# Performance work log

Hardware: AMD Instinct MI355X
Metric: run time of the kernel (lower is better)

The kernel has to match this reference:

```python
import jax, jax.numpy as jnp
import numpy as np

NUM_HEADS = 16
HEAD_DIM = 64
EMBED_DIM = 1024
BSZ = 4
SEQ = 2048


def setup_inputs() -> dict:
    key = jax.random.key(0)
    ks = jax.random.split(key, 6)
    scale = 1.0 / np.sqrt(EMBED_DIM)
    return {
        "x": jax.random.normal(ks[0], (BSZ, SEQ, EMBED_DIM), jnp.float32),
        "rel_pos_bias": jax.random.normal(ks[1], (1, NUM_HEADS, SEQ, SEQ), jnp.float32),
        "Wq": jax.random.normal(ks[2], (EMBED_DIM, EMBED_DIM), jnp.float32) * scale,
        "Wk": jax.random.normal(ks[3], (EMBED_DIM, EMBED_DIM), jnp.float32) * scale,
        "Wv": jax.random.normal(ks[4], (EMBED_DIM, EMBED_DIM), jnp.float32) * scale,
        "Wo": jax.random.normal(ks[5], (EMBED_DIM, EMBED_DIM), jnp.float32) * scale,
    }


def reference(x, rel_pos_bias, Wq, Wk, Wv, Wo):
    b, s, e = x.shape
    h, d = NUM_HEADS, HEAD_DIM
    # projections (T5 linears have no bias); torch Linear: x @ W.T
    q = (x @ Wq.T).reshape(b, s, h, d).transpose(0, 2, 1, 3)  # [b,h,s,d]
    k = (x @ Wk.T).reshape(b, s, h, d).transpose(0, 2, 1, 3)
    v = (x @ Wv.T).reshape(b, s, h, d).transpose(0, 2, 1, 3)
    # unscaled attention scores + additive relative-position bias
    scores = jnp.einsum("bhqd,bhkd->bhqk", q, k) + rel_pos_bias  # [b,h,s,s]
    weights = jax.nn.softmax(scores.astype(jnp.float32), axis=-1).astype(scores.dtype)
    attn = jnp.einsum("bhqk,bhkd->bhqd", weights, v)  # [b,h,s,d]
    attn = attn.transpose(0, 2, 1, 3).reshape(b, s, e)
    return attn @ Wo.T
```

## Files before the change

kernel.cpp:

```cpp
#include <hip/hip_runtime.h>
#include <hip/hip_bf16.h>

#define NH 16
#define HD 64
#define ED 1024
#define BS 4
#define SL 2048

typedef _Float16 f16x8 __attribute__((ext_vector_type(8)));
typedef _Float16 f16x4 __attribute__((ext_vector_type(4)));
typedef _Float16 f16x2 __attribute__((ext_vector_type(2)));
typedef float floatx4 __attribute__((ext_vector_type(4)));

__global__ __launch_bounds__(256) void cvtw_kernel(const float* __restrict__ Wq,
                                                   const float* __restrict__ Wk,
                                                   const float* __restrict__ Wv,
                                                   _Float16* __restrict__ Wh)
{
    const float* W = (blockIdx.y == 0) ? Wq : (blockIdx.y == 1) ? Wk : Wv;
    _Float16* out = Wh + (size_t)blockIdx.y * (ED * ED);
    const int i = (blockIdx.x * 256 + threadIdx.x) * 4;
    float4 v = *(const float4*)(W + i);
    f16x4 c;
    c[0] = (_Float16)v.x; c[1] = (_Float16)v.y;
    c[2] = (_Float16)v.z; c[3] = (_Float16)v.w;
    *(f16x4*)(out + i) = c;
}

__device__ __forceinline__ int lds_boff(int kq, int rc)
{
    return (((kq << 7) + rc) << 4) ^ (kq << 5);
}

template <int A_MODE, int B_MODE, int OUT_MODE>
__device__ __forceinline__ void gemm128_body(const float* __restrict__ Af,
                                             const _Float16* __restrict__ Ah,
                                             const float* __restrict__ Bf,
                                             const _Float16* __restrict__ Bh,
                                             _Float16* __restrict__ outH,
                                             float* __restrict__ outF,
                                             int K, int N)
{
    __shared__ __align__(16) _Float16 As[4 * 128 * 8];
    __shared__ __align__(16) _Float16 Bs[4 * 128 * 8];

    const int tid  = threadIdx.x;
    const int wave = tid >> 6;
    const int lane = tid & 63;
    const int lo16 = lane & 15;
    const int hi4  = lane >> 4;
    const int wm = wave >> 1;
    const int wn = wave & 1;
    const int rowTile = blockIdx.y * 128;
    const int colTile = blockIdx.x * 128;

    floatx4 acc[4][4];
#pragma unroll
    for (int m = 0; m < 4; m++)
#pragma unroll
        for (int n = 0; n < 4; n++)
            acc[m][n] = (floatx4){0.f, 0.f, 0.f, 0.f};

    for (int kb = 0; kb < K; kb += 32) {
        float4 aF[4]; f16x8 aH[2];
        if (A_MODE == 0) {
#pragma unroll
            for (int r = 0; r < 4; r++) {
                const int t2 = tid + r * 256;
                const int row = t2 >> 3;
                const int k4 = (t2 & 7) * 4;
                aF[r] = *(const float4*)(Af + (size_t)(rowTile + row) * K + kb + k4);
            }
        } else {
#pragma unroll
            for (int r = 0; r < 2; r++) {
                const int t2 = tid + r * 256;
                const int row = t2 >> 2;
                const int ko = (t2 & 3) * 8;
                const int gr = rowTile + row;
                const int b = gr >> 11;
                const int s = gr & (SL - 1);
                const int k0 = kb + ko;
                const int h = k0 >> 6;
                const int d = k0 & (HD - 1);
                aH[r] = *(const f16x8*)(Ah + (((size_t)(b * NH + h)) * SL + s) * HD + d);
            }
        }
        f16x8 bH[2]; float4 bF[4];
        if (B_MODE == 0) {
#pragma unroll
            for (int r = 0; r < 2; r++) {
                const int t2 = tid + r * 256;
                const int col = t2 >> 2;
                const int ko = (t2 & 3) * 8;
                bH[r] = *(const f16x8*)(Bh + (size_t)(colTile + col) * K + kb + ko);
            }
        } else {
#pragma unroll
            for (int r = 0; r < 4; r++) {
                const int t2 = tid + r * 256;
                const int col = t2 >> 3;
                const int k4 = (t2 & 7) * 4;
                bF[r] = *(const float4*)(Bf + (size_t)(colTile + col) * K + kb + k4);
            }
        }

        __syncthreads();
        if (A_MODE == 0) {
#pragma unroll
            for (int r = 0; r < 4; r++) {
                const int t2 = tid + r * 256;
                const int row = t2 >> 3;
                const int k4 = (t2 & 7) * 4;
                f16x4 c;
                c[0] = (_Float16)aF[r].x; c[1] = (_Float16)aF[r].y;
                c[2] = (_Float16)aF[r].z; c[3] = (_Float16)aF[r].w;
                *(f16x4*)((char*)As + lds_boff(k4 >> 3, row) + (k4 & 7) * 2) = c;
            }
        } else {
#pragma unroll
            for (int r = 0; r < 2; r++) {
                const int t2 = tid + r * 256;
                const int row = t2 >> 2;
                const int ko = (t2 & 3) * 8;
                *(f16x8*)((char*)As + lds_boff(ko >> 3, row)) = aH[r];
            }
        }
        if (B_MODE == 0) {
#pragma unroll
            for (int r = 0; r < 2; r++) {
                const int t2 = tid + r * 256;
                const int col = t2 >> 2;
                const int ko = (t2 & 3) * 8;
                *(f16x8*)((char*)Bs + lds_boff(ko >> 3, col)) = bH[r];
            }
        } else {
#pragma unroll
            for (int r = 0; r < 4; r++) {
                const int t2 = tid + r * 256;
                const int col = t2 >> 3;
                const int k4 = (t2 & 7) * 4;
                f16x4 c;
                c[0] = (_Float16)bF[r].x; c[1] = (_Float16)bF[r].y;
                c[2] = (_Float16)bF[r].z; c[3] = (_Float16)bF[r].w;
                *(f16x4*)((char*)Bs + lds_boff(k4 >> 3, col) + (k4 & 7) * 2) = c;
            }
        }
        __syncthreads();

        f16x8 af[4], bfr[4];
#pragma unroll
        for (int m = 0; m < 4; m++)
            af[m] = *(const f16x8*)((char*)As + lds_boff(hi4, wm * 64 + m * 16 + lo16));
#pragma unroll
        for (int n = 0; n < 4; n++)
            bfr[n] = *(const f16x8*)((char*)Bs + lds_boff(hi4, wn * 64 + n * 16 + lo16));
#pragma unroll
        for (int m = 0; m < 4; m++)
#pragma unroll
            for (int n = 0; n < 4; n++)
                acc[m][n] = __builtin_amdgcn_mfma_f32_16x16x32_f16(af[m], bfr[n], acc[m][n], 0, 0, 0);
    }

#pragma unroll
    for (int m = 0; m < 4; m++) {
#pragma unroll
        for (int n = 0; n < 4; n++) {
            const int col = colTile + wn * 64 + n * 16 + lo16;
#pragma unroll
            for (int i = 0; i < 4; i++) {
                const int row = rowTile + wm * 64 + m * 16 + hi4 * 4 + i;
                float v = acc[m][n][i];
                if (OUT_MODE == 0) {
                    int b = row >> 11;
                    int s = row & (SL - 1);
                    int h = col >> 6;
                    int d = col & (HD - 1);
                    outH[(((size_t)(b * NH + h)) * SL + s) * HD + d] = (_Float16)v;
                } else {
                    outF[(size_t)row * N + col] = v;
                }
            }
        }
    }
}

__global__ __launch_bounds__(256) void qkv_kernel(const float* __restrict__ x,
                                                  const _Float16* __restrict__ Wh,
                                                  _Float16* __restrict__ Q,
                                                  _Float16* __restrict__ Kk,
                                                  _Float16* __restrict__ V)
{
    const _Float16* W = Wh + (size_t)blockIdx.z * (ED * ED);
    _Float16* out = (blockIdx.z == 0) ? Q : (blockIdx.z == 1) ? Kk : V;
    gemm128_body<0, 0, 0>(x, nullptr, nullptr, W, out, nullptr, ED, ED);
}

__global__ __launch_bounds__(256) void oproj_kernel(const _Float16* __restrict__ A,
                                                    const float* __restrict__ Wo,
                                                    float* __restrict__ out)
{
    gemm128_body<1, 1, 1>(nullptr, A, Wo, nullptr, nullptr, out, ED, ED);
}

__global__ __launch_bounds__(256) void attn_kernel(const _Float16* __restrict__ Qg,
                                                   const _Float16* __restrict__ Kg,
                                                   const _Float16* __restrict__ Vg,
                                                   const float* __restrict__ bias,
                                                   _Float16* __restrict__ attnOut)
{
    __shared__ __align__(16) _Float16 Ks[8 * 64 * 8];
    __shared__ __align__(16) _Float16 Vt[64 * 64];
    __shared__ __align__(16) _Float16 Ps[4 * 32 * 64];
    __shared__ __align__(16) _Float16 Bi[128 * 68];

    const int qt = blockIdx.x;
    const int b  = blockIdx.y;
    const int h  = blockIdx.z;
    const int bh = b * NH + h;
    const int tid  = threadIdx.x;
    const int wave = tid >> 6;
    const int lane = tid & 63;
    const int lo16 = lane & 15;
    const int hi4  = lane >> 4;

    const _Float16* Qbh = Qg + (size_t)bh * SL * HD;
    const _Float16* Kbh = Kg + (size_t)bh * SL * HD;
    const _Float16* Vbh = Vg + (size_t)bh * SL * HD;
    const float* biasH = bias + (size_t)h * SL * SL;

    const int q0 = qt * 128 + wave * 32;

    f16x8 qf[2][2];
#pragma unroll
    for (int m = 0; m < 2; m++)
#pragma unroll
        for (int ks = 0; ks < 2; ks++)
            qf[m][ks] = *(const f16x8*)(Qbh + (size_t)(q0 + m * 16 + lo16) * HD
                                        + ks * 32 + hi4 * 8);

    floatx4 oAcc[2][4];
    float mRow[2][4], lRow[2][4];
#pragma unroll
    for (int m = 0; m < 2; m++)
#pragma unroll
        for (int n = 0; n < 4; n++)
            oAcc[m][n] = (floatx4){0.f, 0.f, 0.f, 0.f};
#pragma unroll
    for (int m = 0; m < 2; m++)
#pragma unroll
        for (int r = 0; r < 4; r++) { mRow[m][r] = -1e30f; lRow[m][r] = 0.f; }

    const int kKey = tid >> 2;
    const int kD0  = (tid & 3) * 8;
    _Float16* kDst0 = Ks + (((kKey >> 4)     ) * 64 + (kKey & 15) + 16 * (kD0 >> 3)) * 8;
    _Float16* kDst1 = Ks + (((kKey >> 4) + 4) * 64 + (kKey & 15) + 16 * (kD0 >> 3)) * 8;
    const int vK0 = (tid >> 3) * 2;
    const int vD0 = (tid & 7) * 8;

    const int bRow = tid >> 4;
    const int bCol = (tid & 15) * 4;
    const float* bThr = biasH + ((size_t)(qt * 128) + bRow) * SL + bCol;

    f16x8 ka = *(const f16x8*)(Kbh + (size_t)(0 + kKey) * HD + kD0);
    f16x8 kb = *(const f16x8*)(Kbh + (size_t)(0 + kKey) * HD + kD0 + 32);
    f16x8 va = *(const f16x8*)(Vbh + (size_t)(0 + vK0    ) * HD + vD0);
    f16x8 vb = *(const f16x8*)(Vbh + (size_t)(0 + vK0 + 1) * HD + vD0);

    for (int kc = 0; kc < SL; kc += 64) {
        float4 bld[8];
#pragma unroll
        for (int r = 0; r < 8; r++)
            bld[r] = *(const float4*)(bThr + (size_t)r * 16 * SL + kc);

        __syncthreads();
        *(f16x8*)kDst0 = ka;
        *(f16x8*)kDst1 = kb;
#pragma unroll
        for (int i = 0; i < 8; i++) {
            const int d = vD0 + i;
            const int sw = (d & 7) ^ ((d >> 3) & 7);
            char* p = (char*)Vt + (d << 7)
                      + ((((vK0 >> 3) ^ sw) & 7) << 4) + ((vK0 & 7) << 1);
            f16x2 pr; pr[0] = va[i]; pr[1] = vb[i];
            *(f16x2*)p = pr;
        }
#pragma unroll
        for (int r = 0; r < 8; r++) {
            f16x4 c;
            c[0] = (_Float16)bld[r].x; c[1] = (_Float16)bld[r].y;
            c[2] = (_Float16)bld[r].z; c[3] = (_Float16)bld[r].w;
            *(f16x4*)(Bi + (bRow + r * 16) * 68 + bCol) = c;
        }
        __syncthreads();

        {
            const int kn = (kc + 64 < SL) ? kc + 64 : kc;
            ka = *(const f16x8*)(Kbh + (size_t)(kn + kKey) * HD + kD0);
            kb = *(const f16x8*)(Kbh + (size_t)(kn + kKey) * HD + kD0 + 32);
            va = *(const f16x8*)(Vbh + (size_t)(kn + vK0    ) * HD + vD0);
            vb = *(const f16x8*)(Vbh + (size_t)(kn + vK0 + 1) * HD + vD0);
        }

        floatx4 s[2][4];
#pragma unroll
        for (int m = 0; m < 2; m++)
#pragma unroll
            for (int n = 0; n < 4; n++)
                s[m][n] = (floatx4){0.f, 0.f, 0.f, 0.f};
        __builtin_amdgcn_s_setprio(1);
#pragma unroll
        for (int ks = 0; ks < 2; ks++)
#pragma unroll
            for (int n = 0; n < 4; n++) {
                f16x8 kf = *(const f16x8*)(Ks + ((ks * 4 + n) * 64 + lane) * 8);
                s[0][n] = __builtin_amdgcn_mfma_f32_16x16x32_f16(qf[0][ks], kf, s[0][n], 0, 0, 0);
                s[1][n] = __builtin_amdgcn_mfma_f32_16x16x32_f16(qf[1][ks], kf, s[1][n], 0, 0, 0);
            }
        __builtin_amdgcn_s_setprio(0);

#pragma unroll
        for (int m = 0; m < 2; m++)
#pragma unroll
            for (int r = 0; r < 4; r++) {
                const int ql = m * 16 + hi4 * 4 + r;
                const _Float16* bsr = Bi + (wave * 32 + ql) * 68;
                float s0 = s[m][0][r] + (float)bsr[lo16];
                float s1 = s[m][1][r] + (float)bsr[16 + lo16];
                float s2 = s[m][2][r] + (float)bsr[32 + lo16];
                float s3 = s[m][3][r] + (float)bsr[48 + lo16];
                float rmax = fmaxf(fmaxf(s0, s1), fmaxf(s2, s3));
                rmax = fmaxf(rmax, __shfl_xor(rmax, 1));
                rmax = fmaxf(rmax, __shfl_xor(rmax, 2));
                rmax = fmaxf(rmax, __shfl_xor(rmax, 4));
                rmax = fmaxf(rmax, __shfl_xor(rmax, 8));
                float mCur = mRow[m][r];
                if (rmax > mCur + 8.f) {
                    const float alpha = __expf(mCur - rmax);
                    mCur = rmax;
                    mRow[m][r] = rmax;
                    lRow[m][r] *= alpha;
#pragma unroll
                    for (int n = 0; n < 4; n++) oAcc[m][n][r] *= alpha;
                }
                float p0 = __expf(s0 - mCur);
                float p1 = __expf(s1 - mCur);
                float p2 = __expf(s2 - mCur);
                float p3 = __expf(s3 - mCur);
                float rsum = (p0 + p1) + (p2 + p3);
                rsum += __shfl_xor(rsum, 1);
                rsum += __shfl_xor(rsum, 2);
                rsum += __shfl_xor(rsum, 4);
                rsum += __shfl_xor(rsum, 8);
                lRow[m][r] += rsum;

                char* pb = (char*)Ps + (wave << 12) + (ql << 7) + ((lo16 & 7) << 1);
                const int kb3 = lo16 >> 3;
                const int swp = (ql & 7) ^ (((ql >> 3) & 3) << 1);
                *(_Float16*)(pb + ((((0 + kb3) ^ swp) & 7) << 4)) = (_Float16)p0;
                *(_Float16*)(pb + ((((2 + kb3) ^ swp) & 7) << 4)) = (_Float16)p1;
                *(_Float16*)(pb + ((((4 + kb3) ^ swp) & 7) << 4)) = (_Float16)p2;
                *(_Float16*)(pb + ((((6 + kb3) ^ swp) & 7) << 4)) = (_Float16)p3;
            }

        __builtin_amdgcn_s_setprio(1);
#pragma unroll
        for (int ks = 0; ks < 2; ks++) {
            f16x8 pa[2];
#pragma unroll
            for (int m = 0; m < 2; m++) {
                const int qlr = m * 16 + lo16;
                const int swp = (qlr & 7) ^ (((qlr >> 3) & 3) << 1);
                pa[m] = *(const f16x8*)((char*)Ps + (wave << 12) + (qlr << 7)
                                        + ((((ks * 4 + hi4) ^ swp) & 7) << 4));
            }
#pragma unroll
            for (int n = 0; n < 4; n++) {
                const int dv = n * 16 + lo16;
                const int swv = (dv & 7) ^ ((dv >> 3) & 7);
                f16x8 vf = *(const f16x8*)((char*)Vt + (dv << 7)
                                           + ((((ks * 4 + hi4) ^ swv) & 7) << 4));
                oAcc[0][n] = __builtin_amdgcn_mfma_f32_16x16x32_f16(pa[0], vf, oAcc[0][n], 0, 0, 0);
                oAcc[1][n] = __builtin_amdgcn_mfma_f32_16x16x32_f16(pa[1], vf, oAcc[1][n], 0, 0, 0);
            }
        }
        __builtin_amdgcn_s_setprio(0);
    }

#pragma unroll
    for (int m = 0; m < 2; m++)
#pragma unroll
        for (int r = 0; r < 4; r++) {
            const float inv = 1.f / lRow[m][r];
            const int q = q0 + m * 16 + hi4 * 4 + r;
#pragma unroll
            for (int n = 0; n < 4; n++)
                attnOut[((size_t)bh * SL + q) * HD + n * 16 + lo16] =
                    (_Float16)(oAcc[m][n][r] * inv);
        }
}

extern "C" void kernel_launch(void* const* d_in, const int* in_sizes, int n_in,
                              void* d_out, int out_size, void* d_ws, size_t ws_size,
                              hipStream_t stream)
{
    (void)in_sizes; (void)n_in; (void)out_size; (void)ws_size;

    const float* x    = (const float*)d_in[0];
    const float* bias = (const float*)d_in[1];
    const float* Wq   = (const float*)d_in[2];
    const float* Wk   = (const float*)d_in[3];
    const float* Wv   = (const float*)d_in[4];
    const float* Wo   = (const float*)d_in[5];

    const size_t nQKV = (size_t)BS * NH * SL * HD;
    _Float16* Qh = (_Float16*)d_out;
    _Float16* Kh = Qh + nQKV;
    _Float16* Vh = (_Float16*)d_ws;
    _Float16* slotB = Vh + nQKV;
    _Float16* Wh = slotB;
    _Float16* attnH = slotB;

    cvtw_kernel<<<dim3(ED * ED / 1024, 3), 256, 0, stream>>>(Wq, Wk, Wv, Wh);

    dim3 gq(ED / 128, (BS * SL) / 128, 3);
    qkv_kernel<<<gq, 256, 0, stream>>>(x, Wh, Qh, Kh, Vh);

    dim3 ga(SL / 128, BS, NH);
    attn_kernel<<<ga, 256, 0, stream>>>(Qh, Kh, Vh, bias, attnH);

    dim3 go(ED / 128, (BS * SL) / 128);
    oproj_kernel<<<go, 256, 0, stream>>>(attnH, Wo, (float*)d_out);
}
```

Measured before the change: 753.5 us.

## Transpose attention MFMAs so each lane owns a query row, double-buffer K/V

Swaps the MFMA operand order so score and output tiles come out transposed, leaving each lane holding one query row. Row max and sum then need only two cross-lane shuffles instead of four per row, and the bias is read straight from global memory into registers rather than staged through shared memory as fp16. K and V shared tiles are double-buffered, which drops one barrier per iteration. The trade-offs are uncoalesced-ish per-lane bias loads with less latency hiding, and more shared memory for the second buffer.

```diff
diff --git a/kernel.cpp b/kernel.cpp
--- a/kernel.cpp
+++ b/kernel.cpp
@@ -209,10 +209,9 @@
                                                    const float* __restrict__ bias,
                                                    _Float16* __restrict__ attnOut)
 {
-    __shared__ __align__(16) _Float16 Ks[8 * 64 * 8];
-    __shared__ __align__(16) _Float16 Vt[64 * 64];
+    __shared__ __align__(16) _Float16 Ks[2][8 * 64 * 8];
+    __shared__ __align__(16) _Float16 Vt[2][64 * 64];
     __shared__ __align__(16) _Float16 Ps[4 * 32 * 64];
-    __shared__ __align__(16) _Float16 Bi[128 * 68];
 
     const int qt = blockIdx.x;
     const int b  = blockIdx.y;
@@ -233,64 +232,54 @@
 
     f16x8 qf[2][2];
 #pragma unroll
-    for (int m = 0; m < 2; m++)
+    for (int nq = 0; nq < 2; nq++)
 #pragma unroll
         for (int ks = 0; ks < 2; ks++)
-            qf[m][ks] = *(const f16x8*)(Qbh + (size_t)(q0 + m * 16 + lo16) * HD
-                                        + ks * 32 + hi4 * 8);
-
-    floatx4 oAcc[2][4];
-    float mRow[2][4], lRow[2][4];
-#pragma unroll
-    for (int m = 0; m < 2; m++)
-#pragma unroll
-        for (int n = 0; n < 4; n++)
-            oAcc[m][n] = (floatx4){0.f, 0.f, 0.f, 0.f};
-#pragma unroll
-    for (int m = 0; m < 2; m++)
-#pragma unroll
-        for (int r = 0; r < 4; r++) { mRow[m][r] = -1e30f; lRow[m][r] = 0.f; }
+            qf[nq][ks] = *(const f16x8*)(Qbh + (size_t)(q0 + nq * 16 + lo16) * HD
+                                         + ks * 32 + hi4 * 8);
+
+    floatx4 oT[4][2];
+#pragma unroll
+    for (int m = 0; m < 4; m++)
+#pragma unroll
+        for (int nq = 0; nq < 2; nq++)
+            oT[m][nq] = (floatx4){0.f, 0.f, 0.f, 0.f};
+    float mRow[2] = {-1e30f, -1e30f};
+    float lRow[2] = {0.f, 0.f};
 
     const int kKey = tid >> 2;
     const int kD0  = (tid & 3) * 8;
-    _Float16* kDst0 = Ks + (((kKey >> 4)     ) * 64 + (kKey & 15) + 16 * (kD0 >> 3)) * 8;
-    _Float16* kDst1 = Ks + (((kKey >> 4) + 4) * 64 + (kKey & 15) + 16 * (kD0 >> 3)) * 8;
+    const int kOff0 = (((kKey >> 4)    ) * 64 + (kKey & 15) + 16 * (kD0 >> 3)) * 8;
+    const int kOff1 = (((kKey >> 4) + 4) * 64 + (kKey & 15) + 16 * (kD0 >> 3)) * 8;
     const int vK0 = (tid >> 3) * 2;
     const int vD0 = (tid & 7) * 8;
 
-    const int bRow = tid >> 4;
-    const int bCol = (tid & 15) * 4;
-    const float* bThr = biasH + ((size_t)(qt * 128) + bRow) * SL + bCol;
-
-    f16x8 ka = *(const f16x8*)(Kbh + (size_t)(0 + kKey) * HD + kD0);
-    f16x8 kb = *(const f16x8*)(Kbh + (size_t)(0 + kKey) * HD + kD0 + 32);
-    f16x8 va = *(const f16x8*)(Vbh + (size_t)(0 + vK0    ) * HD + vD0);
-    f16x8 vb = *(const f16x8*)(Vbh + (size_t)(0 + vK0 + 1) * HD + vD0);
+    const float* bRow0 = biasH + (size_t)(q0 + lo16) * SL + hi4 * 4;
+    const float* bRow1 = biasH + (size_t)(q0 + 16 + lo16) * SL + hi4 * 4;
+
+    const int qA = lo16;
+    const int qB = 16 + lo16;
+    const int swpA = (qA & 7) ^ (((qA >> 3) & 3) << 1);
+    const int swpB = (qB & 7) ^ (((qB >> 3) & 3) << 1);
+    char* psW = (char*)Ps + (wave << 12);
+
+    f16x8 ka = *(const f16x8*)(Kbh + (size_t)(kKey) * HD + kD0);
+    f16x8 kb = *(const f16x8*)(Kbh + (size_t)(kKey) * HD + kD0 + 32);
+    f16x8 va = *(const f16x8*)(Vbh + (size_t)(vK0    ) * HD + vD0);
+    f16x8 vb = *(const f16x8*)(Vbh + (size_t)(vK0 + 1) * HD + vD0);
 
     for (int kc = 0; kc < SL; kc += 64) {
-        float4 bld[8];
-#pragma unroll
-        for (int r = 0; r < 8; r++)
-            bld[r] = *(const float4*)(bThr + (size_t)r * 16 * SL + kc);
-
-        __syncthreads();
-        *(f16x8*)kDst0 = ka;
-        *(f16x8*)kDst1 = kb;
+        const int buf = (kc >> 6) & 1;
+        *(f16x8*)(Ks[buf] + kOff0) = ka;
+        *(f16x8*)(Ks[buf] + kOff1) = kb;
 #pragma unroll
         for (int i = 0; i < 8; i++) {
             const int d = vD0 + i;
             const int sw = (d & 7) ^ ((d >> 3) & 7);
-            char* p = (char*)Vt + (d << 7)
+            char* p = (char*)Vt[buf] + (d << 7)
                       + ((((vK0 >> 3) ^ sw) & 7) << 4) + ((vK0 & 7) << 1);
             f16x2 pr; pr[0] = va[i]; pr[1] = vb[i];
             *(f16x2*)p = pr;
-        }
-#pragma unroll
-        for (int r = 0; r < 8; r++) {
-            f16x4 c;
-            c[0] = (_Float16)bld[r].x; c[1] = (_Float16)bld[r].y;
-            c[2] = (_Float16)bld[r].z; c[3] = (_Float16)bld[r].w;
-            *(f16x4*)(Bi + (bRow + r * 16) * 68 + bCol) = c;
         }
         __syncthreads();
 
@@ -301,103 +290,112 @@
             va = *(const f16x8*)(Vbh + (size_t)(kn + vK0    ) * HD + vD0);
             vb = *(const f16x8*)(Vbh + (size_t)(kn + vK0 + 1) * HD + vD0);
         }
-
-        floatx4 s[2][4];
-#pragma unroll
-        for (int m = 0; m < 2; m++)
-#pragma unroll
-            for (int n = 0; n < 4; n++)
-                s[m][n] = (floatx4){0.f, 0.f, 0.f, 0.f};
+        float4 bb[2][4];
+#pragma unroll
+        for (int mk = 0; mk < 4; mk++) {
+            bb[0][mk] = *(const float4*)(bRow0 + kc + mk * 16);
+            bb[1][mk] = *(const float4*)(bRow1 + kc + mk * 16);
+        }
+
+        floatx4 st[4][2];
+#pragma unroll
+        for (int mk = 0; mk < 4; mk++)
+#pragma unroll
+            for (int nq = 0; nq < 2; nq++)
+                st[mk][nq] = (floatx4){0.f, 0.f, 0.f, 0.f};
         __builtin_amdgcn_s_setprio(1);
 #pragma unroll
         for (int ks = 0; ks < 2; ks++)
 #pragma unroll
-            for (int n = 0; n < 4; n++) {
-                f16x8 kf = *(const f16x8*)(Ks + ((ks * 4 + n) * 64 + lane) * 8);
-                s[0][n] = __builtin_amdgcn_mfma_f32_16x16x32_f16(qf[0][ks], kf, s[0][n], 0, 0, 0);
-                s[1][n] = __builtin_amdgcn_mfma_f32_16x16x32_f16(qf[1][ks], kf, s[1][n], 0, 0, 0);
+            for (int mk = 0; mk < 4; mk++) {
+                f16x8 kf = *(const f16x8*)(Ks[buf] + ((ks * 4 + mk) * 64 + lane) * 8);
+                st[mk][0] = __builtin_amdgcn_mfma_f32_16x16x32_f16(kf, qf[0][ks], st[mk][0], 0, 0, 0);
+                st[mk][1] = __builtin_amdgcn_mfma_f32_16x16x32_f16(kf, qf[1][ks], st[mk][1], 0, 0, 0);
             }
         __builtin_amdgcn_s_setprio(0);
 
 #pragma unroll
-        for (int m = 0; m < 2; m++)
-#pragma unroll
-            for (int r = 0; r < 4; r++) {
-                const int ql = m * 16 + hi4 * 4 + r;
-                const _Float16* bsr = Bi + (wave * 32 + ql) * 68;
-                float s0 = s[m][0][r] + (float)bsr[lo16];
-                float s1 = s[m][1][r] + (float)bsr[16 + lo16];
-                float s2 = s[m][2][r] + (float)bsr[32 + lo16];
-                float s3 = s[m][3][r] + (float)bsr[48 + lo16];
-                float rmax = fmaxf(fmaxf(s0, s1), fmaxf(s2, s3));
-                rmax = fmaxf(rmax, __shfl_xor(rmax, 1));
-                rmax = fmaxf(rmax, __shfl_xor(rmax, 2));
-                rmax = fmaxf(rmax, __shfl_xor(rmax, 4));
-                rmax = fmaxf(rmax, __shfl_xor(rmax, 8));
-                float mCur = mRow[m][r];
-                if (rmax > mCur + 8.f) {
-                    const float alpha = __expf(mCur - rmax);
-                    mCur = rmax;
-                    mRow[m][r] = rmax;
-                    lRow[m][r] *= alpha;
-#pragma unroll
-                    for (int n = 0; n < 4; n++) oAcc[m][n][r] *= alpha;
+        for (int nq = 0; nq < 2; nq++) {
+            float rmax = -1e30f;
+#pragma unroll
+            for (int mk = 0; mk < 4; mk++)
+#pragma unroll
+                for (int r = 0; r < 4; r++) {
+                    float v = st[mk][nq][r] +
+                              ((const float*)&bb[nq][mk])[r];
+                    st[mk][nq][r] = v;
+                    rmax = fmaxf(rmax, v);
                 }
-                float p0 = __expf(s0 - mCur);
-                float p1 = __expf(s1 - mCur);
-                float p2 = __expf(s2 - mCur);
-                float p3 = __expf(s3 - mCur);
-                float rsum = (p0 + p1) + (p2 + p3);
-                rsum += __shfl_xor(rsum, 1);
-                rsum += __shfl_xor(rsum, 2);
-                rsum += __shfl_xor(rsum, 4);
-                rsum += __shfl_xor(rsum, 8);
-                lRow[m][r] += rsum;
-
-                char* pb = (char*)Ps + (wave << 12) + (ql << 7) + ((lo16 & 7) << 1);
-                const int kb3 = lo16 >> 3;
-                const int swp = (ql & 7) ^ (((ql >> 3) & 3) << 1);
-                *(_Float16*)(pb + ((((0 + kb3) ^ swp) & 7) << 4)) = (_Float16)p0;
-                *(_Float16*)(pb + ((((2 + kb3) ^ swp) & 7) << 4)) = (_Float16)p1;
-                *(_Float16*)(pb + ((((4 + kb3) ^ swp) & 7) << 4)) = (_Float16)p2;
-                *(_Float16*)(pb + ((((6 + kb3) ^ swp) & 7) << 4)) = (_Float16)p3;
-            }
+            rmax = fmaxf(rmax, __shfl_xor(rmax, 16));
+            rmax = fmaxf(rmax, __shfl_xor(rmax, 32));
+            float mCur = mRow[nq];
+            if (rmax > mCur + 8.f) {
+                const float al = __expf(mCur - rmax);
+                lRow[nq] *= al;
+#pragma unroll
+                for (int m = 0; m < 4; m++)
+#pragma unroll
+                    for (int i = 0; i < 4; i++) oT[m][nq][i] *= al;
+                mCur = rmax;
+                mRow[nq] = rmax;
+            }
+            float rsum = 0.f;
+#pragma unroll
+            for (int mk = 0; mk < 4; mk++)
+#pragma unroll
+                for (int r = 0; r < 4; r++) {
+                    float e = __expf(st[mk][nq][r] - mCur);
+                    st[mk][nq][r] = e;
+                    rsum += e;
+                }
+            rsum += __shfl_xor(rsum, 16);
+            rsum += __shfl_xor(rsum, 32);
+            lRow[nq] += rsum;
+
+            const int qv  = nq ? qB : qA;
+            const int swp = nq ? swpB : swpA;
+            char* pb = psW + (qv << 7) + ((hi4 & 1) << 3);
+#pragma unroll
+            for (int mk = 0; mk < 4; mk++) {
+                const int oct = mk * 2 + (hi4 >> 1);
+                f16x4 pc;
+#pragma unroll
+                for (int r = 0; r < 4; r++) pc[r] = (_Float16)st[mk][nq][r];
+                *(f16x4*)(pb + (((oct ^ swp) & 7) << 4)) = pc;
+            }
+        }
 
         __builtin_amdgcn_s_setprio(1);
 #pragma unroll
         for (int ks = 0; ks < 2; ks++) {
             f16x8 pa[2];
-#pragma unroll
-            for (int m = 0; m < 2; m++) {
-                const int qlr = m * 16 + lo16;
-                const int swp = (qlr & 7) ^ (((qlr >> 3) & 3) << 1);
-                pa[m] = *(const f16x8*)((char*)Ps + (wave << 12) + (qlr << 7)
-                                        + ((((ks * 4 + hi4) ^ swp) & 7) << 4));
-            }
-#pragma unroll
-            for (int n = 0; n < 4; n++) {
-                const int dv = n * 16 + lo16;
+            pa[0] = *(const f16x8*)(psW + (qA << 7) + ((((ks * 4 + hi4) ^ swpA) & 7) << 4));
+            pa[1] = *(const f16x8*)(psW + (qB << 7) + ((((ks * 4 + hi4) ^ swpB) & 7) << 4));
+#pragma unroll
+            for (int m = 0; m < 4; m++) {
+                const int dv = m * 16 + lo16;
                 const int swv = (dv & 7) ^ ((dv >> 3) & 7);
-                f16x8 vf = *(const f16x8*)((char*)Vt + (dv << 7)
+                f16x8 vf = *(const f16x8*)((char*)Vt[buf] + (dv << 7)
                                            + ((((ks * 4 + hi4) ^ swv) & 7) << 4));
-                oAcc[0][n] = __builtin_amdgcn_mfma_f32_16x16x32_f16(pa[0], vf, oAcc[0][n], 0, 0, 0);
-                oAcc[1][n] = __builtin_amdgcn_mfma_f32_16x16x32_f16(pa[1], vf, oAcc[1][n], 0, 0, 0);
+                oT[m][0] = __builtin_amdgcn_mfma_f32_16x16x32_f16(vf, pa[0], oT[m][0], 0, 0, 0);
+                oT[m][1] = __builtin_amdgcn_mfma_f32_16x16x32_f16(vf, pa[1], oT[m][1], 0, 0, 0);
             }
         }
         __builtin_amdgcn_s_setprio(0);
     }
 
 #pragma unroll
-    for (int m = 0; m < 2; m++)
-#pragma unroll
-        for (int r = 0; r < 4; r++) {
-            const float inv = 1.f / lRow[m][r];
-            const int q = q0 + m * 16 + hi4 * 4 + r;
-#pragma unroll
-            for (int n = 0; n < 4; n++)
-                attnOut[((size_t)bh * SL + q) * HD + n * 16 + lo16] =
-                    (_Float16)(oAcc[m][n][r] * inv);
-        }
+    for (int nq = 0; nq < 2; nq++) {
+        const float inv = 1.f / lRow[nq];
+        const int q = q0 + nq * 16 + lo16;
+#pragma unroll
+        for (int m = 0; m < 4; m++) {
+            f16x4 o4;
+#pragma unroll
+            for (int i = 0; i < 4; i++) o4[i] = (_Float16)(oT[m][nq][i] * inv);
+            *(f16x4*)(attnOut + ((size_t)bh * SL + q) * HD + m * 16 + hi4 * 4) = o4;
+        }
+    }
 }
 
 extern "C" void kernel_launch(void* const* d_in, const int* in_sizes, int n_in,
```

New measurement: 643.2 us. -14.6%, faster.
